# Kernel optimization log

Measured on AMD Instinct MI355X. Metric: run time of the kernel, lower is better.

Reference implementation:

```python
import jax, jax.numpy as jnp
import numpy as np

D_MODEL = 1024
NUM_HEADS = 16
MAX_SEQ_LEN = 2048
THETA = 10000.0
D_K = D_MODEL // NUM_HEADS


def setup_inputs() -> dict:
    key = jax.random.key(0)
    ks = jax.random.split(key, 5)
    x = jax.random.normal(ks[0], (2, 2048, D_MODEL), dtype=jnp.float32)
    token_positions = jnp.arange(2048, dtype=jnp.int32)
    s = 1.0 / np.sqrt(D_MODEL)
    w_q = jax.random.normal(ks[1], (D_MODEL, D_MODEL), dtype=jnp.float32) * s
    w_k = jax.random.normal(ks[2], (D_MODEL, D_MODEL), dtype=jnp.float32) * s
    w_v = jax.random.normal(ks[3], (D_MODEL, D_MODEL), dtype=jnp.float32) * s
    w_o = jax.random.normal(ks[4], (D_MODEL, D_MODEL), dtype=jnp.float32) * s
    return {"x": x, "token_positions": token_positions,
            "w_q": w_q, "w_k": w_k, "w_v": w_v, "w_o": w_o}


def _rope_tables():
    inv_freq = 1.0 / (THETA ** (jnp.arange(0, D_K, 2, dtype=jnp.float32) / D_K))
    angles = jnp.arange(MAX_SEQ_LEN, dtype=jnp.float32)[:, None] * inv_freq[None, :]
    return jnp.cos(angles), jnp.sin(angles)  # [max_seq_len, d_k//2]


def _apply_rope(x, cos, sin):
    # x: [..., s, d_k]; interleaved-pair rotation, cos/sin: [s, d_k//2]
    x0 = x[..., 0::2]
    x1 = x[..., 1::2]
    y0 = x0 * cos - x1 * sin
    y1 = x0 * sin + x1 * cos
    return jnp.stack((y0, y1), axis=-1).reshape(x.shape)


def reference(x, token_positions, w_q, w_k, w_v, w_o):
    b, s, _ = x.shape
    h, dk = NUM_HEADS, D_K
    # torch Linear: y = x @ W^T
    q = (x @ w_q.T).reshape(b, s, h, dk).transpose(0, 2, 1, 3)  # [b,h,s,dk]
    k = (x @ w_k.T).reshape(b, s, h, dk).transpose(0, 2, 1, 3)
    v = (x @ w_v.T).reshape(b, s, h, dk).transpose(0, 2, 1, 3)
    cos_c, sin_c = _rope_tables()
    cos = cos_c[token_positions]  # [s, dk//2]
    sin = sin_c[token_positions]
    q = _apply_rope(q, cos, sin)
    k = _apply_rope(k, cos, sin)
    scores = jnp.einsum('bhqd,bhkd->bhqk', q, k) / jnp.sqrt(jnp.float32(dk))
    causal = jnp.tril(jnp.ones((s, s), dtype=bool))
    scores = jnp.where(causal, scores, -jnp.inf)
    attn = jax.nn.softmax(scores, axis=-1)
    out = jnp.einsum('bhqk,bhkd->bhqd', attn, v)
    out = out.transpose(0, 2, 1, 3).reshape(b, s, h * dk)
    return out @ w_o.T
```

## Files before the change

### kernel.cpp

```cpp
#include <hip/hip_runtime.h>
#include <cstdint>
#include <cstddef>

#define DEV static __device__ __forceinline__

typedef __attribute__((ext_vector_type(8))) short bf16x8;
typedef __attribute__((ext_vector_type(4))) float f32x4;

DEV uint16_t f2bf(float f) {
  uint32_t u = __builtin_bit_cast(uint32_t, f);
  u += 0x7FFFu + ((u >> 16) & 1u);
  return (uint16_t)(u >> 16);
}

DEV uint32_t packbf(float a, float b) {
  return (__builtin_bit_cast(uint32_t, a) >> 16) |
         (__builtin_bit_cast(uint32_t, b) & 0xFFFF0000u);
}

DEV float fexp2(float x) { return __builtin_amdgcn_exp2f(x); }

template <int CTRL>
DEV float dppf(float v) {
  return __builtin_bit_cast(
      float, __builtin_amdgcn_update_dpp(0, __builtin_bit_cast(int, v), CTRL, 0xF, 0xF, true));
}

DEV float swz16(float v) {
  return __builtin_bit_cast(
      float, __builtin_amdgcn_ds_swizzle(__builtin_bit_cast(int, v), 0x401F));
}
DEV float bperm(int lane_idx, float v) {
  return __builtin_bit_cast(
      float, __builtin_amdgcn_ds_bpermute(lane_idx << 2, __builtin_bit_cast(int, v)));
}

DEV void load_lds16(const void* g, void* l) {
  auto gp = reinterpret_cast<const uint32_t __attribute__((address_space(1)))*>(
      reinterpret_cast<uintptr_t>(g));
  auto lp = reinterpret_cast<uint32_t __attribute__((address_space(3)))*>(
      reinterpret_cast<uintptr_t>(l));
  __builtin_amdgcn_global_load_lds(gp, lp, 16, 0, 0);
}

__global__ __launch_bounds__(256) void cvt_all(const float* __restrict__ x,
                                               const float* __restrict__ wq,
                                               const float* __restrict__ wk,
                                               const float* __restrict__ wv,
                                               const float* __restrict__ wo,
                                               const int* __restrict__ tokpos,
                                               uint16_t* __restrict__ dst,
                                               float2* __restrict__ rtab) {
  int bx = blockIdx.x;
  if (bx >= 8192) {
    int idx = (bx - 8192) * 256 + threadIdx.x;
    int s = idx >> 5, f = idx & 31;
    float invf = __expf(-0.28782314f * (float)f);
    float pos = (float)tokpos[s];
    float sn, cs;
    __sincosf(pos * invf, &sn, &cs);
    rtab[idx] = make_float2(cs, sn);
    return;
  }
  int gi = bx * 1024 + threadIdx.x * 4;
  const float* s;
  int li;
  if (gi < 4194304) {
    s = x; li = gi;
  } else {
    int j = gi - 4194304;
    int r = j >> 20;
    li = j & 1048575;
    s = (r == 0) ? wq : (r == 1) ? wk : (r == 2) ? wv : wo;
  }
  float4 v = *reinterpret_cast<const float4*>(s + li);
  ushort4 o;
  o.x = f2bf(v.x); o.y = f2bf(v.y); o.z = f2bf(v.z); o.w = f2bf(v.w);
  *reinterpret_cast<ushort4*>(dst + gi) = o;
}

__global__ __launch_bounds__(512) void gemm_qkv(const uint16_t* __restrict__ A,
                                                const uint16_t* __restrict__ Wqkv,
                                                uint16_t* __restrict__ QK,
                                                uint16_t* __restrict__ VTb,
                                                const float2* __restrict__ rtab) {
  __shared__ union {
    struct { uint16_t a[2][128 * 64]; uint16_t b[2][128 * 64]; } st;
    uint16_t t[128 * 128];
  } sm;

  const int tid = threadIdx.x;
  const int lane = tid & 63, w = tid >> 6;
  const int q = lane >> 4, l16 = lane & 15;
  const int wm = w >> 1, wn = w & 1;

  const int orig = blockIdx.y * 24 + blockIdx.x;
  const int logical = (orig & 7) * 96 + (orig >> 3);
  const int bm = logical / 24, bn = logical % 24;
  const int wsel = bn >> 3;

  const f32x4 z4 = {0.f, 0.f, 0.f, 0.f};
  f32x4 acc[2][4];
#pragma unroll
  for (int i = 0; i < 2; ++i)
#pragma unroll
    for (int j = 0; j < 4; ++j) acc[i][j] = z4;

  const int srow = tid >> 3, sslot = tid & 7;
  const uint16_t* Ab = A + (size_t)bm * 128 * 1024;
  const uint16_t* Bb = Wqkv + (size_t)bn * 128 * 1024;

  auto stage = [&](int buf, int k0) {
#pragma unroll
    for (int is = 0; is < 2; ++is) {
      int row = is * 64 + srow;
      int gch = sslot ^ (row & 7);
      char* la = (char*)sm.st.a[buf] + (is * 64 + w * 8) * 128;
      char* lb = (char*)sm.st.b[buf] + (is * 64 + w * 8) * 128;
      load_lds16(Ab + (size_t)row * 1024 + k0 + gch * 8, la);
      load_lds16(Bb + (size_t)row * 1024 + k0 + gch * 8, lb);
    }
  };

  stage(0, 0);
  for (int t = 0; t < 16; ++t) {
    const int cur = t & 1;
    __syncthreads();
    if (t + 1 < 16) stage(cur ^ 1, (t + 1) * 64);
#pragma unroll
    for (int ks = 0; ks < 2; ++ks) {
      bf16x8 af[2], bfr[4];
#pragma unroll
      for (int i = 0; i < 2; ++i) {
        int ra = wm * 32 + i * 16 + l16;
        af[i] = *reinterpret_cast<const bf16x8*>(sm.st.a[cur] + ra * 64 +
                                                 (((ks * 4 + q) ^ (ra & 7)) * 8));
      }
#pragma unroll
      for (int j = 0; j < 4; ++j) {
        int rb = wn * 64 + j * 16 + l16;
        bfr[j] = *reinterpret_cast<const bf16x8*>(sm.st.b[cur] + rb * 64 +
                                                  (((ks * 4 + q) ^ (rb & 7)) * 8));
      }
#pragma unroll
      for (int i = 0; i < 2; ++i)
#pragma unroll
        for (int j = 0; j < 4; ++j)
          acc[i][j] =
              __builtin_amdgcn_mfma_f32_16x16x32_bf16(af[i], bfr[j], acc[i][j], 0, 0, 0);
    }
  }

  if (wsel < 2) {
    uint16_t* O = QK + (size_t)wsel * 4194304;
    const float scq = (wsel == 0) ? 0.18033688f : 1.0f;
#pragma unroll
    for (int j = 0; j < 4; ++j) {
      int gn = bn * 128 + wn * 64 + j * 16 + l16;
      int cn = gn & 1023;
      int f = (gn & 63) >> 1;
      float sgn = (lane & 1) ? 1.f : -1.f;
#pragma unroll
      for (int i = 0; i < 2; ++i) {
#pragma unroll
        for (int r = 0; r < 4; ++r) {
          int gm = bm * 128 + wm * 32 + i * 16 + q * 4 + r;
          float2 cssn = rtab[(gm & 2047) * 32 + f];
          float v = acc[i][j][r];
          float o = dppf<0xB1>(v);
          O[(size_t)gm * 1024 + cn] = f2bf((v * cssn.x + sgn * o * cssn.y) * scq);
        }
      }
    }
  } else {
    const int bnv = bn & 7;
    __syncthreads();
#pragma unroll
    for (int i = 0; i < 2; ++i)
#pragma unroll
      for (int j = 0; j < 4; ++j)
#pragma unroll
        for (int r = 0; r < 4; ++r) {
          int mL = wm * 32 + i * 16 + q * 4 + r;
          int nL = wn * 64 + j * 16 + l16;
          int ch = (mL >> 3) ^ (nL & 15);
          sm.t[nL * 128 + ch * 8 + (mL & 7)] = f2bf(acc[i][j][r]);
        }
    __syncthreads();
    const int b = (bm * 128) >> 11;
    const int sblk = (bm * 128) & 2047;
#pragma unroll
    for (int it = 0; it < 4; ++it) {
      int nL = it * 32 + (tid >> 4);
      int mch = tid & 15;
      int slot = mch ^ (nL & 15);
      bf16x8 vv = *reinterpret_cast<const bf16x8*>(sm.t + nL * 128 + slot * 8);
      int gn = bnv * 128 + nL;
      int h = gn >> 6, d = gn & 63;
      *reinterpret_cast<bf16x8*>(VTb + ((size_t)((b * 16 + h) * 64 + d)) * 2048 + sblk +
                                 mch * 8) = vv;
    }
  }
}

__global__ __launch_bounds__(512) void gemm_out(const uint16_t* __restrict__ A,
                                                const uint16_t* __restrict__ Bw,
                                                float* __restrict__ O) {
  __shared__ uint16_t sa[2][128 * 64];
  __shared__ uint16_t sb[2][64 * 64];

  const int tid = threadIdx.x;
  const int lane = tid & 63, w = tid >> 6;
  const int q = lane >> 4, l16 = lane & 15;
  const int wm = w >> 1, wn = w & 1;

  const int orig = blockIdx.y * 16 + blockIdx.x;
  const int logical = (orig & 7) * 64 + (orig >> 3);
  const int bm = logical / 16, bn = logical % 16;

  const f32x4 z4 = {0.f, 0.f, 0.f, 0.f};
  f32x4 acc[2][2];
#pragma unroll
  for (int i = 0; i < 2; ++i)
#pragma unroll
    for (int j = 0; j < 2; ++j) acc[i][j] = z4;

  const int srow = tid >> 3, sslot = tid & 7;
  const uint16_t* Ab = A + (size_t)bm * 128 * 1024;
  const uint16_t* Bb = Bw + (size_t)bn * 64 * 1024;

  auto stage = [&](int buf, int k0) {
#pragma unroll
    for (int is = 0; is < 2; ++is) {
      int row = is * 64 + srow;
      int gch = sslot ^ (row & 7);
      load_lds16(Ab + (size_t)row * 1024 + k0 + gch * 8,
                 (char*)sa[buf] + (is * 64 + w * 8) * 128);
    }
    {
      int row = srow;
      int gch = sslot ^ (row & 7);
      load_lds16(Bb + (size_t)row * 1024 + k0 + gch * 8,
                 (char*)sb[buf] + (w * 8) * 128);
    }
  };

  stage(0, 0);
  for (int t = 0; t < 16; ++t) {
    const int cur = t & 1;
    __syncthreads();
    if (t + 1 < 16) stage(cur ^ 1, (t + 1) * 64);
#pragma unroll
    for (int ks = 0; ks < 2; ++ks) {
      bf16x8 af[2], bfr[2];
#pragma unroll
      for (int i = 0; i < 2; ++i) {
        int ra = wm * 32 + i * 16 + l16;
        af[i] = *reinterpret_cast<const bf16x8*>(sa[cur] + ra * 64 +
                                                 (((ks * 4 + q) ^ (ra & 7)) * 8));
      }
#pragma unroll
      for (int j = 0; j < 2; ++j) {
        int rb = wn * 32 + j * 16 + l16;
        bfr[j] = *reinterpret_cast<const bf16x8*>(sb[cur] + rb * 64 +
                                                  (((ks * 4 + q) ^ (rb & 7)) * 8));
      }
#pragma unroll
      for (int i = 0; i < 2; ++i)
#pragma unroll
        for (int j = 0; j < 2; ++j)
          acc[i][j] =
              __builtin_amdgcn_mfma_f32_16x16x32_bf16(af[i], bfr[j], acc[i][j], 0, 0, 0);
    }
  }

#pragma unroll
  for (int i = 0; i < 2; ++i)
#pragma unroll
    for (int r = 0; r < 4; ++r) {
      int gm = bm * 128 + wm * 32 + i * 16 + q * 4 + r;
#pragma unroll
      for (int j = 0; j < 2; ++j) {
        int gn = bn * 64 + wn * 32 + j * 16 + l16;
        O[(size_t)gm * 1024 + gn] = acc[i][j][r];
      }
    }
}

__global__ __launch_bounds__(512) void flash_attn(const uint16_t* __restrict__ Q,
                                                  const uint16_t* __restrict__ K,
                                                  const uint16_t* __restrict__ VT,
                                                  uint16_t* __restrict__ AO) {
  __shared__ uint16_t ksm[2][128 * 64];
  __shared__ uint16_t vsm[2][64 * 128];
  __shared__ uint16_t psm[8][16 * 128];

  const int tid = threadIdx.x;
  const int lane = tid & 63, w = tid >> 6;
  const int q = lane >> 4, l16 = lane & 15;

  const int orig = blockIdx.y * 8 + blockIdx.x;
  const int logical = (orig & 7) * 32 + (orig >> 3);
  const int p = logical & 7;
  const int bh = logical >> 3;
  const int b = bh >> 4, h = bh & 15;

  const size_t baseBS = (size_t)b * 2048 * 1024 + h * 64;
  const size_t baseVT = (size_t)bh * 64 * 2048;
  uint16_t* pw = psm[w];
  const f32x4 z4 = {0.f, 0.f, 0.f, 0.f};

  auto stage = [&](int buf, int kt) {
#pragma unroll
    for (int is = 0; is < 2; ++is) {
      int row = is * 64 + (tid >> 3);
      int gch = (tid & 7) ^ (row & 7);
      load_lds16(K + baseBS + (size_t)(kt * 128 + row) * 1024 + gch * 8,
                 (char*)ksm[buf] + (is * 64 + w * 8) * 128);
    }
#pragma unroll
    for (int is = 0; is < 2; ++is) {
      int row = is * 32 + (tid >> 4);
      int gch = (tid & 15) ^ (row & 15);
      load_lds16(VT + baseVT + (size_t)row * 2048 + kt * 128 + gch * 8,
                 (char*)vsm[buf] + (is * 32 + w * 4) * 256);
    }
  };

  for (int t = 0; t < 2; ++t) {
    const int qt = t ? (15 - p) : p;
    const int r0 = qt * 128 + w * 16;
    const int nkt = qt + 1;

    bf16x8 qf[2];
#pragma unroll
    for (int ks = 0; ks < 2; ++ks)
      qf[ks] = *reinterpret_cast<const bf16x8*>(
          Q + baseBS + (size_t)(r0 + l16) * 1024 + ks * 32 + q * 8);

    f32x4 oa[4];
#pragma unroll
    for (int di = 0; di < 4; ++di) oa[di] = z4;
    float m2 = -1e30f, li = 0.f;

    __syncthreads();
    stage(0, 0);

    for (int kt = 0; kt < nkt; ++kt) {
      const int cur = kt & 1;
      __syncthreads();
      if (kt + 1 < nkt) stage(cur ^ 1, kt + 1);

      f32x4 sc[8];
#pragma unroll
      for (int nj = 0; nj < 8; ++nj) sc[nj] = z4;
#pragma unroll
      for (int ks = 0; ks < 2; ++ks) {
        bf16x8 kf[8];
#pragma unroll
        for (int nj = 0; nj < 8; ++nj) {
          int rk = nj * 16 + l16;
          kf[nj] = *reinterpret_cast<const bf16x8*>(ksm[cur] + rk * 64 +
                                                    (((ks * 4 + q) ^ (rk & 7)) * 8));
        }
        __builtin_amdgcn_s_setprio(1);
#pragma unroll
        for (int nj = 0; nj < 8; ++nj)
          sc[nj] =
              __builtin_amdgcn_mfma_f32_16x16x32_bf16(kf[nj], qf[ks], sc[nj], 0, 0, 0);
        __builtin_amdgcn_s_setprio(0);
      }

      if (kt == nkt - 1) {
#pragma unroll
        for (int nj = 0; nj < 8; ++nj)
#pragma unroll
          for (int r = 0; r < 4; ++r) {
            int col = nj * 16 + q * 4 + r;
            int row = w * 16 + l16;
            if (col > row) sc[nj][r] = -1e30f;
          }
      }

      f32x4 m4 = sc[0];
#pragma unroll
      for (int nj = 1; nj < 8; ++nj) {
#pragma unroll
        for (int r = 0; r < 4; ++r) m4[r] = fmaxf(m4[r], sc[nj][r]);
      }
      float pmax = fmaxf(fmaxf(m4[0], m4[1]), fmaxf(m4[2], m4[3]));
      pmax = fmaxf(pmax, swz16(pmax));
      pmax = fmaxf(pmax, bperm(lane ^ 32, pmax));

      if (__any(pmax > m2 + 8.f)) {
        float mn = fmaxf(m2, pmax);
        float al = fexp2(m2 - mn);
        m2 = mn;
        li *= al;
        float ar[4];
#pragma unroll
        for (int r = 0; r < 4; ++r)
          ar[r] = bperm((lane & 48) | (q * 4 + r), al);
#pragma unroll
        for (int di = 0; di < 4; ++di)
#pragma unroll
          for (int r = 0; r < 4; ++r) oa[di][r] *= ar[r];
      }

      {
        uint16_t* pwr = pw + l16 * 128 + (q & 1) * 4;
        const int swz = l16 & 15;
#pragma unroll
        for (int nj = 0; nj < 8; ++nj) {
          float e0 = fexp2(sc[nj][0] - m2);
          float e1 = fexp2(sc[nj][1] - m2);
          float e2 = fexp2(sc[nj][2] - m2);
          float e3 = fexp2(sc[nj][3] - m2);
          li += (e0 + e1) + (e2 + e3);
          uint64_t pk = (uint64_t)packbf(e0, e1) | ((uint64_t)packbf(e2, e3) << 32);
          *reinterpret_cast<uint64_t*>(
              pwr + (((nj * 2 + (q >> 1)) ^ swz) * 8)) = pk;
        }
      }

#pragma unroll
      for (int ks = 0; ks < 4; ++ks) {
        bf16x8 pf;
        {
          int pr = l16;
          pf = *reinterpret_cast<const bf16x8*>(pw + pr * 128 +
                                                (((ks * 4 + q) ^ (pr & 15)) * 8));
        }
        bf16x8 vf[4];
#pragma unroll
        for (int di = 0; di < 4; ++di) {
          int vr = di * 16 + l16;
          vf[di] = *reinterpret_cast<const bf16x8*>(vsm[cur] + vr * 128 +
                                                    (((ks * 4 + q) ^ (vr & 15)) * 8));
        }
        __builtin_amdgcn_s_setprio(1);
#pragma unroll
        for (int di = 0; di < 4; ++di)
          oa[di] =
              __builtin_amdgcn_mfma_f32_16x16x32_bf16(pf, vf[di], oa[di], 0, 0, 0);
        __builtin_amdgcn_s_setprio(0);
      }
    }

    float lf = li;
    lf += swz16(lf);
    lf += bperm(lane ^ 32, lf);
    float invL = 1.f / lf;
    float inv_r[4];
#pragma unroll
    for (int r = 0; r < 4; ++r)
      inv_r[r] = bperm((lane & 48) | (q * 4 + r), invL);
#pragma unroll
    for (int r = 0; r < 4; ++r) {
      int gm = r0 + q * 4 + r;
#pragma unroll
      for (int di = 0; di < 4; ++di)
        AO[baseBS + (size_t)gm * 1024 + di * 16 + l16] = f2bf(oa[di][r] * inv_r[r]);
    }
  }
}

extern "C" void kernel_launch(void* const* d_in, const int* in_sizes, int n_in,
                              void* d_out, int out_size, void* d_ws, size_t ws_size,
                              hipStream_t stream) {
  (void)in_sizes; (void)n_in; (void)out_size; (void)ws_size;
  const float* x = (const float*)d_in[0];
  const int* tokpos = (const int*)d_in[1];
  const float* wq = (const float*)d_in[2];
  const float* wk = (const float*)d_in[3];
  const float* wv = (const float*)d_in[4];
  const float* wo = (const float*)d_in[5];
  float* out = (float*)d_out;

  uint16_t* ws = (uint16_t*)d_ws;
  uint16_t* xb = ws;
  uint16_t* wqb = xb + 4194304;
  uint16_t* wob = wqb + 3145728;
  uint16_t* Qb = wob + 1048576;
  uint16_t* VTb = Qb + 8388608;
  uint16_t* AOb = VTb + 4194304;
  float2* rtab = (float2*)AOb;

  cvt_all<<<8448, 256, 0, stream>>>(x, wq, wk, wv, wo, tokpos, xb, rtab);

  gemm_qkv<<<dim3(24, 32), 512, 0, stream>>>(xb, wqb, Qb, VTb, rtab);

  flash_attn<<<dim3(8, 32), 512, 0, stream>>>(Qb, Qb + 4194304, VTb, AOb);

  gemm_out<<<dim3(16, 32), 512, 0, stream>>>(AOb, wob, out);
}
```

Before: 166.5 us.

## Process paired causal query tiles together to share staged K/V tiles

The attention kernel used to handle its two query tiles (p and 15-p) one after the other, staging K/V from global memory separately for each. Now both query tiles are processed in a single pass over key tiles, so each staged K/V tile is reused by both tiles and total global loads and barriers drop. The cost is holding two sets of accumulators and Q fragments in registers, which may lower occupancy or cause spills. The shorter tile also finishes early, leaving its work unevenly spread across iterations. There is also a possible hazard: the P scratch buffer pw is shared by both tile_body calls, and only a wave-local ordering protects the second write from overlapping the first one's reads.

```diff
diff --git a/kernel.cpp b/kernel.cpp
--- a/kernel.cpp
+++ b/kernel.cpp
@@ -327,126 +327,129 @@
     }
   };
 
-  for (int t = 0; t < 2; ++t) {
-    const int qt = t ? (15 - p) : p;
-    const int r0 = qt * 128 + w * 16;
-    const int nkt = qt + 1;
-
-    bf16x8 qf[2];
-#pragma unroll
-    for (int ks = 0; ks < 2; ++ks)
-      qf[ks] = *reinterpret_cast<const bf16x8*>(
-          Q + baseBS + (size_t)(r0 + l16) * 1024 + ks * 32 + q * 8);
-
-    f32x4 oa[4];
-#pragma unroll
-    for (int di = 0; di < 4; ++di) oa[di] = z4;
-    float m2 = -1e30f, li = 0.f;
-
+  const int qtA = p, qtB = 15 - p;
+  const int nkt = qtB + 1;
+
+  bf16x8 qfA[2], qfB[2];
+#pragma unroll
+  for (int ks = 0; ks < 2; ++ks) {
+    qfA[ks] = *reinterpret_cast<const bf16x8*>(
+        Q + baseBS + (size_t)(qtA * 128 + w * 16 + l16) * 1024 + ks * 32 + q * 8);
+    qfB[ks] = *reinterpret_cast<const bf16x8*>(
+        Q + baseBS + (size_t)(qtB * 128 + w * 16 + l16) * 1024 + ks * 32 + q * 8);
+  }
+
+  f32x4 oaA[4], oaB[4];
+#pragma unroll
+  for (int di = 0; di < 4; ++di) { oaA[di] = z4; oaB[di] = z4; }
+  float m2A = -1e30f, liA = 0.f, m2B = -1e30f, liB = 0.f;
+
+  auto tile_body = [&](int cur, const bf16x8 (&qf)[2], f32x4 (&oa)[4],
+                       float& m2, float& li, bool diag) {
+    f32x4 sc[8];
+#pragma unroll
+    for (int nj = 0; nj < 8; ++nj) sc[nj] = z4;
+#pragma unroll
+    for (int ks = 0; ks < 2; ++ks) {
+      bf16x8 kf[8];
+#pragma unroll
+      for (int nj = 0; nj < 8; ++nj) {
+        int rk = nj * 16 + l16;
+        kf[nj] = *reinterpret_cast<const bf16x8*>(ksm[cur] + rk * 64 +
+                                                  (((ks * 4 + q) ^ (rk & 7)) * 8));
+      }
+      __builtin_amdgcn_s_setprio(1);
+#pragma unroll
+      for (int nj = 0; nj < 8; ++nj)
+        sc[nj] =
+            __builtin_amdgcn_mfma_f32_16x16x32_bf16(kf[nj], qf[ks], sc[nj], 0, 0, 0);
+      __builtin_amdgcn_s_setprio(0);
+    }
+
+    if (diag) {
+#pragma unroll
+      for (int nj = 0; nj < 8; ++nj)
+#pragma unroll
+        for (int r = 0; r < 4; ++r) {
+          int col = nj * 16 + q * 4 + r;
+          int row = w * 16 + l16;
+          if (col > row) sc[nj][r] = -1e30f;
+        }
+    }
+
+    f32x4 m4 = sc[0];
+#pragma unroll
+    for (int nj = 1; nj < 8; ++nj) {
+#pragma unroll
+      for (int r = 0; r < 4; ++r) m4[r] = fmaxf(m4[r], sc[nj][r]);
+    }
+    float pmax = fmaxf(fmaxf(m4[0], m4[1]), fmaxf(m4[2], m4[3]));
+    pmax = fmaxf(pmax, swz16(pmax));
+    pmax = fmaxf(pmax, bperm(lane ^ 32, pmax));
+
+    if (__any(pmax > m2 + 8.f)) {
+      float mn = fmaxf(m2, pmax);
+      float al = fexp2(m2 - mn);
+      m2 = mn;
+      li *= al;
+      float ar[4];
+#pragma unroll
+      for (int r = 0; r < 4; ++r)
+        ar[r] = bperm((lane & 48) | (q * 4 + r), al);
+#pragma unroll
+      for (int di = 0; di < 4; ++di)
+#pragma unroll
+        for (int r = 0; r < 4; ++r) oa[di][r] *= ar[r];
+    }
+
+    {
+      uint16_t* pwr = pw + l16 * 128 + (q & 1) * 4;
+      const int swz = l16 & 15;
+#pragma unroll
+      for (int nj = 0; nj < 8; ++nj) {
+        float e0 = fexp2(sc[nj][0] - m2);
+        float e1 = fexp2(sc[nj][1] - m2);
+        float e2 = fexp2(sc[nj][2] - m2);
+        float e3 = fexp2(sc[nj][3] - m2);
+        li += (e0 + e1) + (e2 + e3);
+        uint64_t pk = (uint64_t)packbf(e0, e1) | ((uint64_t)packbf(e2, e3) << 32);
+        *reinterpret_cast<uint64_t*>(
+            pwr + (((nj * 2 + (q >> 1)) ^ swz) * 8)) = pk;
+      }
+    }
+
+#pragma unroll
+    for (int ks = 0; ks < 4; ++ks) {
+      bf16x8 pf = *reinterpret_cast<const bf16x8*>(pw + l16 * 128 +
+                                                   (((ks * 4 + q) ^ (l16 & 15)) * 8));
+      bf16x8 vf[4];
+#pragma unroll
+      for (int di = 0; di < 4; ++di) {
+        int vr = di * 16 + l16;
+        vf[di] = *reinterpret_cast<const bf16x8*>(vsm[cur] + vr * 128 +
+                                                  (((ks * 4 + q) ^ (vr & 15)) * 8));
+      }
+      __builtin_amdgcn_s_setprio(1);
+#pragma unroll
+      for (int di = 0; di < 4; ++di)
+        oa[di] =
+            __builtin_amdgcn_mfma_f32_16x16x32_bf16(pf, vf[di], oa[di], 0, 0, 0);
+      __builtin_amdgcn_s_setprio(0);
+    }
+  };
+
+  stage(0, 0);
+
+  for (int kt = 0; kt < nkt; ++kt) {
+    const int cur = kt & 1;
     __syncthreads();
-    stage(0, 0);
-
-    for (int kt = 0; kt < nkt; ++kt) {
-      const int cur = kt & 1;
-      __syncthreads();
-      if (kt + 1 < nkt) stage(cur ^ 1, kt + 1);
-
-      f32x4 sc[8];
-#pragma unroll
-      for (int nj = 0; nj < 8; ++nj) sc[nj] = z4;
-#pragma unroll
-      for (int ks = 0; ks < 2; ++ks) {
-        bf16x8 kf[8];
-#pragma unroll
-        for (int nj = 0; nj < 8; ++nj) {
-          int rk = nj * 16 + l16;
-          kf[nj] = *reinterpret_cast<const bf16x8*>(ksm[cur] + rk * 64 +
-                                                    (((ks * 4 + q) ^ (rk & 7)) * 8));
-        }
-        __builtin_amdgcn_s_setprio(1);
-#pragma unroll
-        for (int nj = 0; nj < 8; ++nj)
-          sc[nj] =
-              __builtin_amdgcn_mfma_f32_16x16x32_bf16(kf[nj], qf[ks], sc[nj], 0, 0, 0);
-        __builtin_amdgcn_s_setprio(0);
-      }
-
-      if (kt == nkt - 1) {
-#pragma unroll
-        for (int nj = 0; nj < 8; ++nj)
-#pragma unroll
-          for (int r = 0; r < 4; ++r) {
-            int col = nj * 16 + q * 4 + r;
-            int row = w * 16 + l16;
-            if (col > row) sc[nj][r] = -1e30f;
-          }
-      }
-
-      f32x4 m4 = sc[0];
-#pragma unroll
-      for (int nj = 1; nj < 8; ++nj) {
-#pragma unroll
-        for (int r = 0; r < 4; ++r) m4[r] = fmaxf(m4[r], sc[nj][r]);
-      }
-      float pmax = fmaxf(fmaxf(m4[0], m4[1]), fmaxf(m4[2], m4[3]));
-      pmax = fmaxf(pmax, swz16(pmax));
-      pmax = fmaxf(pmax, bperm(lane ^ 32, pmax));
-
-      if (__any(pmax > m2 + 8.f)) {
-        float mn = fmaxf(m2, pmax);
-        float al = fexp2(m2 - mn);
-        m2 = mn;
-        li *= al;
-        float ar[4];
-#pragma unroll
-        for (int r = 0; r < 4; ++r)
-          ar[r] = bperm((lane & 48) | (q * 4 + r), al);
-#pragma unroll
-        for (int di = 0; di < 4; ++di)
-#pragma unroll
-          for (int r = 0; r < 4; ++r) oa[di][r] *= ar[r];
-      }
-
-      {
-        uint16_t* pwr = pw + l16 * 128 + (q & 1) * 4;
-        const int swz = l16 & 15;
-#pragma unroll
-        for (int nj = 0; nj < 8; ++nj) {
-          float e0 = fexp2(sc[nj][0] - m2);
-          float e1 = fexp2(sc[nj][1] - m2);
-          float e2 = fexp2(sc[nj][2] - m2);
-          float e3 = fexp2(sc[nj][3] - m2);
-          li += (e0 + e1) + (e2 + e3);
-          uint64_t pk = (uint64_t)packbf(e0, e1) | ((uint64_t)packbf(e2, e3) << 32);
-          *reinterpret_cast<uint64_t*>(
-              pwr + (((nj * 2 + (q >> 1)) ^ swz) * 8)) = pk;
-        }
-      }
-
-#pragma unroll
-      for (int ks = 0; ks < 4; ++ks) {
-        bf16x8 pf;
-        {
-          int pr = l16;
-          pf = *reinterpret_cast<const bf16x8*>(pw + pr * 128 +
-                                                (((ks * 4 + q) ^ (pr & 15)) * 8));
-        }
-        bf16x8 vf[4];
-#pragma unroll
-        for (int di = 0; di < 4; ++di) {
-          int vr = di * 16 + l16;
-          vf[di] = *reinterpret_cast<const bf16x8*>(vsm[cur] + vr * 128 +
-                                                    (((ks * 4 + q) ^ (vr & 15)) * 8));
-        }
-        __builtin_amdgcn_s_setprio(1);
-#pragma unroll
-        for (int di = 0; di < 4; ++di)
-          oa[di] =
-              __builtin_amdgcn_mfma_f32_16x16x32_bf16(pf, vf[di], oa[di], 0, 0, 0);
-        __builtin_amdgcn_s_setprio(0);
-      }
-    }
-
+    if (kt + 1 < nkt) stage(cur ^ 1, kt + 1);
+
+    if (kt <= qtA) tile_body(cur, qfA, oaA, m2A, liA, kt == qtA);
+    tile_body(cur, qfB, oaB, m2B, liB, kt == qtB);
+  }
+
+  auto finalize = [&](int qt, const f32x4 (&oa)[4], float li) {
     float lf = li;
     lf += swz16(lf);
     lf += bperm(lane ^ 32, lf);
@@ -457,12 +460,14 @@
       inv_r[r] = bperm((lane & 48) | (q * 4 + r), invL);
 #pragma unroll
     for (int r = 0; r < 4; ++r) {
-      int gm = r0 + q * 4 + r;
+      int gm = qt * 128 + w * 16 + q * 4 + r;
 #pragma unroll
       for (int di = 0; di < 4; ++di)
         AO[baseBS + (size_t)gm * 1024 + di * 16 + l16] = f2bf(oa[di][r] * inv_r[r]);
     }
-  }
+  };
+  finalize(qtA, oaA, liA);
+  finalize(qtB, oaB, liB);
 }
 
 extern "C" void kernel_launch(void* const* d_in, const int* in_sizes, int n_in,
```

New measurement: 167.5 us. Within noise of the previous version (+0.7%).
